# Optimization experiments

Hardware: AMD Instinct MI355X
Metric: run time of the kernel (lower is better)

The kernel has to match this reference:

```python
import jax, jax.numpy as jnp
import numpy as np

N_NODES = 100000
N_EDGES = 3200000
IN_CH = 128
HID = 8
HEADS = 8
NEG_SLOPE = 0.2  # PyG GATConv default


def setup_inputs() -> dict:
    key = jax.random.key(0)
    ks = jax.random.split(key, 12)
    s = 0.1
    return {
        "x": jax.random.normal(ks[0], (N_NODES, IN_CH), jnp.float32),
        "edge_index": jax.random.randint(ks[1], (2, N_EDGES), 0, N_NODES, dtype=jnp.int64),
        "W1": jax.random.normal(ks[2], (IN_CH, HEADS * HID), jnp.float32) * s,
        "a_src1": jax.random.normal(ks[3], (1, HEADS, HID), jnp.float32) * s,
        "a_dst1": jax.random.normal(ks[4], (1, HEADS, HID), jnp.float32) * s,
        "b1": jax.random.normal(ks[5], (HEADS * HID,), jnp.float32) * s,
        "W2": jax.random.normal(ks[6], (HEADS * HID, HID), jnp.float32) * s,
        "a_src2": jax.random.normal(ks[7], (1, 1, HID), jnp.float32) * s,
        "a_dst2": jax.random.normal(ks[8], (1, 1, HID), jnp.float32) * s,
        "b2": jax.random.normal(ks[9], (HID,), jnp.float32) * s,
        "Wc": jax.random.normal(ks[10], (HID, 2), jnp.float32) * s,
        "bc": jax.random.normal(ks[11], (2,), jnp.float32) * s,
    }


def gat_conv(x, src, dst, W, a_src, a_dst, b, concat):
    """PyG-style GATConv (eval mode, self-loops already appended to src/dst)."""
    n = x.shape[0]
    H, C = a_src.shape[1], a_src.shape[2]
    h = (x @ W).reshape(n, H, C)                       # [N,H,C]
    alpha_src = jnp.sum(h * a_src, axis=-1)            # [N,H]
    alpha_dst = jnp.sum(h * a_dst, axis=-1)            # [N,H]
    e = jax.nn.leaky_relu(alpha_src[src] + alpha_dst[dst], NEG_SLOPE)  # [E,H]
    # segment softmax over destination-node neighborhoods
    m = jax.ops.segment_max(e, dst, num_segments=n)    # [N,H]
    m = jnp.where(jnp.isfinite(m), m, 0.0)
    p = jnp.exp(e - m[dst])
    z = jax.ops.segment_sum(p, dst, num_segments=n)    # [N,H]
    alpha = p / (z[dst] + 1e-16)                       # [E,H]
    out = jax.ops.segment_sum(alpha[..., None] * h[src], dst, num_segments=n)  # [N,H,C]
    out = out.reshape(n, H * C) if concat else out.mean(axis=1)
    return out + b


def reference(x, edge_index, W1, a_src1, a_dst1, b1, W2, a_src2, a_dst2, b2, Wc, bc):
    n = x.shape[0]
    loops = jnp.arange(n, dtype=edge_index.dtype)
    src = jnp.concatenate([edge_index[0], loops])
    dst = jnp.concatenate([edge_index[1], loops])
    h = jax.nn.relu(gat_conv(x, src, dst, W1, a_src1, a_dst1, b1, concat=True))
    embeddings = gat_conv(h, src, dst, W2, a_src2, a_dst2, b2, concat=False)
    logits = embeddings @ Wc + bc
    return embeddings, logits
```

## Files before the change

### kernel.cpp

```cpp
#include <hip/hip_runtime.h>
#include <hip/hip_bf16.h>
#include <hip/hip_fp16.h>

#define NN 100000
#define IN_CH 128
#define HID 8
#define HEADS 8
#define HC 64
#define BSH 8
#define NBUCK ((NN + 255) >> 8)
#define NBLK 512
#define PCAP 10240
#define LOG2E 1.44269504088896340736f
#define QSCALE (8.0f / 127.0f)
#define QINV   (127.0f / 8.0f)

__device__ __forceinline__ unsigned short f2bf(float f) {
    unsigned u = __float_as_uint(f);
    unsigned r = (u + 0x7fffu + ((u >> 16) & 1u)) >> 16;
    return (unsigned short)r;
}


__global__ __launch_bounds__(256) void k_bincount(const int* __restrict__ ei, int E, int ET,
                                                  int cpb, int* __restrict__ cnt) {
    __shared__ int h[NBUCK];
    for (int i = threadIdx.x; i < NBUCK; i += 256) h[i] = 0;
    __syncthreads();
    int beg = blockIdx.x * cpb, end = min(ET, beg + cpb);
    for (int t = beg + threadIdx.x; t < end; t += 256) {
        int d = (t < E) ? ei[E + t] : (t - E);
        atomicAdd(&h[d >> BSH], 1);
    }
    __syncthreads();
    for (int i = threadIdx.x; i < NBUCK; i += 256) cnt[i * NBLK + blockIdx.x] = h[i];
}

__global__ __launch_bounds__(256) void k_colscan(int* __restrict__ cnt, int* __restrict__ btot) {
    __shared__ int sd[256];
    int t = threadIdx.x;
    int* col = cnt + blockIdx.x * NBLK;
    int v0 = col[2 * t], v1 = col[2 * t + 1];
    int s = v0 + v1;
    sd[t] = s;
    __syncthreads();
    for (int off = 1; off < 256; off <<= 1) {
        int u = (t >= off) ? sd[t - off] : 0;
        __syncthreads();
        sd[t] += u;
        __syncthreads();
    }
    int excl = sd[t] - s;
    col[2 * t] = excl;
    col[2 * t + 1] = excl + v0;
    if (t == 255) btot[blockIdx.x] = excl + s;
}

__global__ __launch_bounds__(256) void k_bucketbase(const int* __restrict__ btot,
                                                    int* __restrict__ bbase,
                                                    int* __restrict__ row_ptr) {
    __shared__ int sd[256];
    int t = threadIdx.x;
    int v0 = (2 * t < NBUCK) ? btot[2 * t] : 0;
    int v1 = (2 * t + 1 < NBUCK) ? btot[2 * t + 1] : 0;
    int s = v0 + v1;
    sd[t] = s;
    __syncthreads();
    for (int off = 1; off < 256; off <<= 1) {
        int u = (t >= off) ? sd[t - off] : 0;
        __syncthreads();
        sd[t] += u;
        __syncthreads();
    }
    int excl = sd[t] - s;
    if (2 * t < NBUCK) bbase[2 * t] = excl;
    if (2 * t + 1 < NBUCK) bbase[2 * t + 1] = excl + v0;
    if (t == 255) { bbase[NBUCK] = excl + s; row_ptr[NN] = excl + s; }
}

__global__ __launch_bounds__(256) void k_binscatter(const int* __restrict__ ei, int E, int ET,
                                                    int cpb, const int* __restrict__ cnt,
                                                    const int* __restrict__ bbase,
                                                    unsigned* __restrict__ pairs) {
    __shared__ int cur[NBUCK];
    for (int i = threadIdx.x; i < NBUCK; i += 256)
        cur[i] = bbase[i] + cnt[i * NBLK + blockIdx.x];
    __syncthreads();
    int beg = blockIdx.x * cpb, end = min(ET, beg + cpb);
    for (int t = beg + threadIdx.x; t < end; t += 256) {
        int s, d;
        if (t < E) { s = ei[t]; d = ei[E + t]; } else { s = t - E; d = t - E; }
        int pos = atomicAdd(&cur[d >> BSH], 1);
        pairs[pos] = ((unsigned)s << 8) | (unsigned)(d & 255);
    }
}

__global__ __launch_bounds__(256) void k_bucketscatter(const unsigned* __restrict__ pairs,
                                                       const int* __restrict__ bbase,
                                                       int* __restrict__ row_ptr,
                                                       int* __restrict__ csr) {
    __shared__ unsigned pl[PCAP];
    __shared__ int h[256];
    __shared__ int sd[256];
    int b = blockIdx.x;
    int t = threadIdx.x;
    int beg = bbase[b], end = bbase[b + 1];
    int cntE = end - beg;
    bool inl = cntE <= PCAP;
    if (inl)
        for (int j = t; j < cntE; j += 256) pl[j] = pairs[beg + j];
    h[t] = 0;
    __syncthreads();
    for (int j = t; j < cntE; j += 256) {
        unsigned pv = inl ? pl[j] : pairs[beg + j];
        atomicAdd(&h[pv & 255u], 1);
    }
    __syncthreads();
    int v = h[t];
    sd[t] = v;
    __syncthreads();
    for (int off = 1; off < 256; off <<= 1) {
        int u = (t >= off) ? sd[t - off] : 0;
        __syncthreads();
        sd[t] += u;
        __syncthreads();
    }
    int excl = sd[t] - v;
    int node = (b << 8) + t;
    if (node < NN) row_ptr[node] = beg + excl;
    __syncthreads();
    h[t] = beg + excl;
    __syncthreads();
    for (int j = t; j < cntE; j += 256) {
        unsigned pv = inl ? pl[j] : pairs[beg + j];
        int pos = atomicAdd(&h[pv & 255u], 1);
        csr[pos] = (int)(pv >> 8);
    }
}


__global__ __launch_bounds__(256) void k_gemm1(const float* __restrict__ x,
                                               const float* __restrict__ W1,
                                               const float* __restrict__ aS,
                                               const float* __restrict__ aD,
                                               unsigned* __restrict__ h1q,
                                               unsigned short* __restrict__ asrc1h,
                                               float* __restrict__ adst1) {
    __shared__ float wl[IN_CH * HC];
    int tid = threadIdx.x;
    {
        const float4* Wg4 = (const float4*)W1;
        float4* wl4 = (float4*)wl;
#pragma unroll
        for (int i = 0; i < 8; ++i) wl4[tid + i * 256] = Wg4[tid + i * 256];
    }
    __syncthreads();
    int lane = tid & 63;
    int wv = tid >> 6;
    int q = lane >> 4;
    int c0 = (lane & 15) * 4;
    int base = blockIdx.x * 64 + wv * 16 + q * 4;
    if (base + 4 > NN) base = NN - 4;
    const float4* xr0 = (const float4*)(x + (size_t)(base + 0) * IN_CH);
    const float4* xr1 = (const float4*)(x + (size_t)(base + 1) * IN_CH);
    const float4* xr2 = (const float4*)(x + (size_t)(base + 2) * IN_CH);
    const float4* xr3 = (const float4*)(x + (size_t)(base + 3) * IN_CH);
    float4 ac0 = make_float4(0.f, 0.f, 0.f, 0.f);
    float4 ac1 = ac0, ac2 = ac0, ac3 = ac0;
#pragma unroll 2
    for (int kq = 0; kq < IN_CH / 4; ++kq) {
        const float4* wrow = (const float4*)(wl + (kq * 4) * HC + c0);
        float4 w0 = wrow[0];
        float4 w1 = wrow[HC / 4];
        float4 w2 = wrow[2 * (HC / 4)];
        float4 w3 = wrow[3 * (HC / 4)];
        float4 xv;
        xv = xr0[kq];
        ac0.x += xv.x * w0.x + xv.y * w1.x + xv.z * w2.x + xv.w * w3.x;
        ac0.y += xv.x * w0.y + xv.y * w1.y + xv.z * w2.y + xv.w * w3.y;
        ac0.z += xv.x * w0.z + xv.y * w1.z + xv.z * w2.z + xv.w * w3.z;
        ac0.w += xv.x * w0.w + xv.y * w1.w + xv.z * w2.w + xv.w * w3.w;
        xv = xr1[kq];
        ac1.x += xv.x * w0.x + xv.y * w1.x + xv.z * w2.x + xv.w * w3.x;
        ac1.y += xv.x * w0.y + xv.y * w1.y + xv.z * w2.y + xv.w * w3.y;
        ac1.z += xv.x * w0.z + xv.y * w1.z + xv.z * w2.z + xv.w * w3.z;
        ac1.w += xv.x * w0.w + xv.y * w1.w + xv.z * w2.w + xv.w * w3.w;
        xv = xr2[kq];
        ac2.x += xv.x * w0.x + xv.y * w1.x + xv.z * w2.x + xv.w * w3.x;
        ac2.y += xv.x * w0.y + xv.y * w1.y + xv.z * w2.y + xv.w * w3.y;
        ac2.z += xv.x * w0.z + xv.y * w1.z + xv.z * w2.z + xv.w * w3.z;
        ac2.w += xv.x * w0.w + xv.y * w1.w + xv.z * w2.w + xv.w * w3.w;
        xv = xr3[kq];
        ac3.x += xv.x * w0.x + xv.y * w1.x + xv.z * w2.x + xv.w * w3.x;
        ac3.y += xv.x * w0.y + xv.y * w1.y + xv.z * w2.y + xv.w * w3.y;
        ac3.z += xv.x * w0.z + xv.y * w1.z + xv.z * w2.z + xv.w * w3.z;
        ac3.w += xv.x * w0.w + xv.y * w1.w + xv.z * w2.w + xv.w * w3.w;
    }
    float4 accs[4] = {ac0, ac1, ac2, ac3};
#pragma unroll
    for (int r = 0; r < 4; ++r) {
        float4 acc = accs[r];
        int row = base + r;
        int q0 = min(max(__float2int_rn(acc.x * QINV) + 128, 0), 255);
        int q1 = min(max(__float2int_rn(acc.y * QINV) + 128, 0), 255);
        int q2 = min(max(__float2int_rn(acc.z * QINV) + 128, 0), 255);
        int q3 = min(max(__float2int_rn(acc.w * QINV) + 128, 0), 255);
        unsigned u = (unsigned)q0 | ((unsigned)q1 << 8) | ((unsigned)q2 << 16) |
                     ((unsigned)q3 << 24);
        h1q[row * 16 + (lane & 15)] = u;
        int head = (lane & 15) >> 1;
        int cl = c0 & 7;
        const float* as = aS + head * 8 + cl;
        const float* ad = aD + head * 8 + cl;
        float ps = acc.x * as[0] + acc.y * as[1] + acc.z * as[2] + acc.w * as[3];
        float pd = acc.x * ad[0] + acc.y * ad[1] + acc.z * ad[2] + acc.w * ad[3];
        ps += __shfl_xor(ps, 1, 64);
        pd += __shfl_xor(pd, 1, 64);
        if ((lane & 1) == 0) {
            asrc1h[row * 8 + head] = __half_as_ushort(__float2half(ps * LOG2E));
            adst1[row * 8 + head] = pd * LOG2E;
        }
    }
}


__global__ __launch_bounds__(256) void k_agg1(const int* __restrict__ row_ptr,
                                              const int* __restrict__ csr,
                                              const unsigned short* __restrict__ asrc1h,
                                              const float* __restrict__ adst1,
                                              const uint2* __restrict__ h1q,
                                              const float* __restrict__ b1,
                                              const float* __restrict__ W2,
                                              const float* __restrict__ aS2,
                                              const float* __restrict__ aD2,
                                              unsigned short* __restrict__ h2bf,
                                              float* __restrict__ asrc2,
                                              float* __restrict__ adst2) {
    int tid = threadIdx.x;
    int lane = tid & 63;
    int slot = lane >> 3;
    int hl = lane & 7;
    float w2r[8];
#pragma unroll
    for (int i = 0; i < 8; ++i) w2r[i] = W2[(hl * 8 + i) * 8 + slot];
    float4 b0 = *(const float4*)(b1 + hl * 8);
    float4 b1v = *(const float4*)(b1 + hl * 8 + 4);
    float as2 = aS2[slot], ad2 = aD2[slot];
    int nbase = (blockIdx.x * 4 + (tid >> 6)) * 4;
    for (int ni = 0; ni < 4; ++ni) {
        int n = nbase + ni;
        float adst = adst1[n * 8 + hl];
        int beg = row_ptr[n], end = row_ptr[n + 1];
        int nit = (end - beg + 7) >> 3;
        float z = 0.f;
        float4 accA = make_float4(0.f, 0.f, 0.f, 0.f);
        float4 accB = make_float4(0.f, 0.f, 0.f, 0.f);
        int j0 = beg + slot;
        bool v0 = j0 < end;
        int s0 = v0 ? csr[j0] : 0;
        int j1 = j0 + 8;
        bool v1 = j1 < end;
        int s1 = v1 ? csr[j1] : 0;
        unsigned short a0 = asrc1h[s0 * 8 + hl];
        uint2 r0 = h1q[s0 * 8 + hl];
        int jn = j1;
        for (int it = 0; it < nit; ++it) {
            int j2 = jn + 8;
            bool v2 = j2 < end;
            int s2 = v2 ? csr[j2] : 0;
            unsigned short a1 = asrc1h[s1 * 8 + hl];
            uint2 r1 = h1q[s1 * 8 + hl];
            float e = __half2float(__ushort_as_half(a0)) + adst;
            e = fmaxf(e, 0.2f * e);
            float p = v0 ? exp2f(e) : 0.f;
            z += p;
            accA.x += p * (float)(r0.x & 255u);
            accA.y += p * (float)((r0.x >> 8) & 255u);
            accA.z += p * (float)((r0.x >> 16) & 255u);
            accA.w += p * (float)(r0.x >> 24);
            accB.x += p * (float)(r0.y & 255u);
            accB.y += p * (float)((r0.y >> 8) & 255u);
            accB.z += p * (float)((r0.y >> 16) & 255u);
            accB.w += p * (float)(r0.y >> 24);
            v0 = v1; a0 = a1; r0 = r1;
            v1 = v2; s1 = s2;
            jn = j2;
        }
#pragma unroll
        for (int off = 8; off <= 32; off <<= 1) {
            z += __shfl_xor(z, off, 64);
            accA.x += __shfl_xor(accA.x, off, 64);
            accA.y += __shfl_xor(accA.y, off, 64);
            accA.z += __shfl_xor(accA.z, off, 64);
            accA.w += __shfl_xor(accA.w, off, 64);
            accB.x += __shfl_xor(accB.x, off, 64);
            accB.y += __shfl_xor(accB.y, off, 64);
            accB.z += __shfl_xor(accB.z, off, 64);
            accB.w += __shfl_xor(accB.w, off, 64);
        }
        float inv = 1.f / (z + 1e-16f);
        float si = QSCALE * inv;
        float zc = 128.f * z;
        float hr0 = fmaxf((accA.x - zc) * si + b0.x, 0.f);
        float hr1 = fmaxf((accA.y - zc) * si + b0.y, 0.f);
        float hr2 = fmaxf((accA.z - zc) * si + b0.z, 0.f);
        float hr3 = fmaxf((accA.w - zc) * si + b0.w, 0.f);
        float hr4 = fmaxf((accB.x - zc) * si + b1v.x, 0.f);
        float hr5 = fmaxf((accB.y - zc) * si + b1v.y, 0.f);
        float hr6 = fmaxf((accB.z - zc) * si + b1v.z, 0.f);
        float hr7 = fmaxf((accB.w - zc) * si + b1v.w, 0.f);
        float part = hr0 * w2r[0] + hr1 * w2r[1] + hr2 * w2r[2] + hr3 * w2r[3] +
                     hr4 * w2r[4] + hr5 * w2r[5] + hr6 * w2r[6] + hr7 * w2r[7];
        part += __shfl_xor(part, 1, 64);
        part += __shfl_xor(part, 2, 64);
        part += __shfl_xor(part, 4, 64);
        if (hl == 0) {
            h2bf[n * 8 + slot] = f2bf(part);
            float s2v = part * as2;
            float d2v = part * ad2;
            s2v += __shfl_xor(s2v, 8, 64);
            s2v += __shfl_xor(s2v, 16, 64);
            s2v += __shfl_xor(s2v, 32, 64);
            d2v += __shfl_xor(d2v, 8, 64);
            d2v += __shfl_xor(d2v, 16, 64);
            d2v += __shfl_xor(d2v, 32, 64);
            if (slot == 0) {
                asrc2[n] = s2v * LOG2E;
                adst2[n] = d2v * LOG2E;
            }
        }
    }
}


__global__ __launch_bounds__(256) void k_agg2(const int* __restrict__ row_ptr,
                                              const int* __restrict__ csr,
                                              const float* __restrict__ asrc2,
                                              const float* __restrict__ adst2,
                                              const unsigned short* __restrict__ h2bf,
                                              const float* __restrict__ b2,
                                              const float* __restrict__ Wc,
                                              const float* __restrict__ bc,
                                              float* __restrict__ out) {
    int tid = threadIdx.x;
    int lane = tid & 63;
    int slot = lane >> 3;
    int sl = lane & 7;
    float b2v = b2[sl];
    float wc0 = Wc[sl * 2 + 0], wc1 = Wc[sl * 2 + 1];
    int nbase = (blockIdx.x * 4 + (tid >> 6)) * 4;
    for (int ni = 0; ni < 4; ++ni) {
        int n = nbase + ni;
        float adst = adst2[n];
        int beg = row_ptr[n], end = row_ptr[n + 1];
        int nit = (end - beg + 7) >> 3;
        float z = 0.f, acc = 0.f;
        int j0 = beg + slot;
        bool v0 = j0 < end;
        int s0 = v0 ? csr[j0] : 0;
        int j1 = j0 + 8;
        bool v1 = j1 < end;
        int s1 = v1 ? csr[j1] : 0;
        float a0 = asrc2[s0];
        unsigned short u0 = h2bf[s0 * 8 + sl];
        int jn = j1;
        for (int it = 0; it < nit; ++it) {
            int j2 = jn + 8;
            bool v2 = j2 < end;
            int s2 = v2 ? csr[j2] : 0;
            float a1 = asrc2[s1];
            unsigned short u1 = h2bf[s1 * 8 + sl];
            float e = a0 + adst;
            e = fmaxf(e, 0.2f * e);
            float p = v0 ? exp2f(e) : 0.f;
            float h0 = __uint_as_float(((unsigned)u0) << 16);
            z += p;
            acc += p * h0;
            v0 = v1; a0 = a1; u0 = u1;
            v1 = v2; s1 = s2;
            jn = j2;
        }
#pragma unroll
        for (int off = 8; off <= 32; off <<= 1) {
            z += __shfl_xor(z, off, 64);
            acc += __shfl_xor(acc, off, 64);
        }
        float emb = acc / (z + 1e-16f) + b2v;
        if (slot == 0) out[(size_t)n * HID + sl] = emb;
        float t0 = emb * wc0;
        float t1 = emb * wc1;
        t0 += __shfl_xor(t0, 1, 64); t0 += __shfl_xor(t0, 2, 64); t0 += __shfl_xor(t0, 4, 64);
        t1 += __shfl_xor(t1, 1, 64); t1 += __shfl_xor(t1, 2, 64); t1 += __shfl_xor(t1, 4, 64);
        if (lane == 0) {
            out[(size_t)NN * HID + n * 2 + 0] = t0 + bc[0];
            out[(size_t)NN * HID + n * 2 + 1] = t1 + bc[1];
        }
    }
}


extern "C" void kernel_launch(void* const* d_in, const int* in_sizes, int n_in,
                              void* d_out, int out_size, void* d_ws, size_t ws_size,
                              hipStream_t stream) {
    const float* x  = (const float*)d_in[0];
    const int*   ei = (const int*)d_in[1];
    const float* W1 = (const float*)d_in[2];
    const float* aS = (const float*)d_in[3];
    const float* aD = (const float*)d_in[4];
    const float* b1 = (const float*)d_in[5];
    const float* W2 = (const float*)d_in[6];
    const float* aS2 = (const float*)d_in[7];
    const float* aD2 = (const float*)d_in[8];
    const float* b2 = (const float*)d_in[9];
    const float* Wc = (const float*)d_in[10];
    const float* bc = (const float*)d_in[11];

    int E = in_sizes[1] / 2;
    int N = NN;
    int ET = E + N;
    int cpb = (ET + NBLK - 1) / NBLK;

    char* p = (char*)d_ws;
    auto alloc = [&](size_t bytes) -> char* {
        char* r = p;
        p += (bytes + 255) & ~(size_t)255;
        return r;
    };
    unsigned* h1q   = (unsigned*)alloc((size_t)N * 16 * 4);
    unsigned short* asrc1h = (unsigned short*)alloc((size_t)N * 8 * 2);
    float* adst1    = (float*)alloc((size_t)N * 8 * 4);
    unsigned short* h2bf = (unsigned short*)alloc((size_t)N * 8 * 2);
    float* asrc2    = (float*)alloc((size_t)N * 4);
    float* adst2    = (float*)alloc((size_t)N * 4);
    int*   row_ptr  = (int*)alloc((size_t)(N + 1) * 4);
    int*   cnt      = (int*)alloc((size_t)NBUCK * NBLK * 4);
    int*   btot     = (int*)alloc((size_t)NBUCK * 4);
    int*   bbase    = (int*)alloc((size_t)(NBUCK + 1) * 4);
    int*   csr      = (int*)alloc((size_t)ET * 4);
    unsigned* pairs = (unsigned*)alloc((size_t)ET * 4);

    k_bincount<<<NBLK, 256, 0, stream>>>(ei, E, ET, cpb, cnt);
    k_colscan<<<NBUCK, 256, 0, stream>>>(cnt, btot);
    k_bucketbase<<<1, 256, 0, stream>>>(btot, bbase, row_ptr);
    k_binscatter<<<NBLK, 256, 0, stream>>>(ei, E, ET, cpb, cnt, bbase, pairs);
    k_bucketscatter<<<NBUCK, 256, 0, stream>>>(pairs, bbase, row_ptr, csr);

    k_gemm1<<<(N + 63) / 64, 256, 0, stream>>>(x, W1, aS, aD, h1q, asrc1h, adst1);
    k_agg1<<<N / 16, 256, 0, stream>>>(row_ptr, csr, asrc1h, adst1,
                                       (const uint2*)h1q, b1, W2, aS2, aD2,
                                       h2bf, asrc2, adst2);
    k_agg2<<<N / 16, 256, 0, stream>>>(row_ptr, csr, asrc2, adst2, h2bf, b2, Wc, bc,
                                       (float*)d_out);
}
```

Measured before the change: 216.3 us.

## Co-schedule GEMM1 blocks with CSR-build kernels and drop validity checks in aggregation

Merges the layer-1 GEMM into the bincount and binscatter kernels as extra blocks, splitting the GEMM rows between the two launches. This lets the compute-bound GEMM overlap the atomic-heavy CSR construction and removes one kernel launch. The shared-memory buffer is reused by both roles, so the bincount/binscatter blocks now reserve the full 32KB GEMM allocation, which may lower their occupancy. Separately, the aggregation loops load sentinel attention scores (-inf half, or -3e38 float) for invalid edges so exp2 yields zero, removing the per-edge validity select.

```diff
diff --git a/kernel.cpp b/kernel.cpp
--- a/kernel.cpp
+++ b/kernel.cpp
@@ -11,6 +11,9 @@
 #define NBUCK ((NN + 255) >> 8)
 #define NBLK 512
 #define PCAP 10240
+#define GB  ((NN + 63) / 64)
+#define GH1 782
+#define GH2 (GB - GH1)
 #define LOG2E 1.44269504088896340736f
 #define QSCALE (8.0f / 127.0f)
 #define QINV   (127.0f / 8.0f)
@@ -22,131 +25,15 @@
 }
 
 
-__global__ __launch_bounds__(256) void k_bincount(const int* __restrict__ ei, int E, int ET,
-                                                  int cpb, int* __restrict__ cnt) {
-    __shared__ int h[NBUCK];
-    for (int i = threadIdx.x; i < NBUCK; i += 256) h[i] = 0;
-    __syncthreads();
-    int beg = blockIdx.x * cpb, end = min(ET, beg + cpb);
-    for (int t = beg + threadIdx.x; t < end; t += 256) {
-        int d = (t < E) ? ei[E + t] : (t - E);
-        atomicAdd(&h[d >> BSH], 1);
-    }
-    __syncthreads();
-    for (int i = threadIdx.x; i < NBUCK; i += 256) cnt[i * NBLK + blockIdx.x] = h[i];
-}
-
-__global__ __launch_bounds__(256) void k_colscan(int* __restrict__ cnt, int* __restrict__ btot) {
-    __shared__ int sd[256];
-    int t = threadIdx.x;
-    int* col = cnt + blockIdx.x * NBLK;
-    int v0 = col[2 * t], v1 = col[2 * t + 1];
-    int s = v0 + v1;
-    sd[t] = s;
-    __syncthreads();
-    for (int off = 1; off < 256; off <<= 1) {
-        int u = (t >= off) ? sd[t - off] : 0;
-        __syncthreads();
-        sd[t] += u;
-        __syncthreads();
-    }
-    int excl = sd[t] - s;
-    col[2 * t] = excl;
-    col[2 * t + 1] = excl + v0;
-    if (t == 255) btot[blockIdx.x] = excl + s;
-}
-
-__global__ __launch_bounds__(256) void k_bucketbase(const int* __restrict__ btot,
-                                                    int* __restrict__ bbase,
-                                                    int* __restrict__ row_ptr) {
-    __shared__ int sd[256];
-    int t = threadIdx.x;
-    int v0 = (2 * t < NBUCK) ? btot[2 * t] : 0;
-    int v1 = (2 * t + 1 < NBUCK) ? btot[2 * t + 1] : 0;
-    int s = v0 + v1;
-    sd[t] = s;
-    __syncthreads();
-    for (int off = 1; off < 256; off <<= 1) {
-        int u = (t >= off) ? sd[t - off] : 0;
-        __syncthreads();
-        sd[t] += u;
-        __syncthreads();
-    }
-    int excl = sd[t] - s;
-    if (2 * t < NBUCK) bbase[2 * t] = excl;
-    if (2 * t + 1 < NBUCK) bbase[2 * t + 1] = excl + v0;
-    if (t == 255) { bbase[NBUCK] = excl + s; row_ptr[NN] = excl + s; }
-}
-
-__global__ __launch_bounds__(256) void k_binscatter(const int* __restrict__ ei, int E, int ET,
-                                                    int cpb, const int* __restrict__ cnt,
-                                                    const int* __restrict__ bbase,
-                                                    unsigned* __restrict__ pairs) {
-    __shared__ int cur[NBUCK];
-    for (int i = threadIdx.x; i < NBUCK; i += 256)
-        cur[i] = bbase[i] + cnt[i * NBLK + blockIdx.x];
-    __syncthreads();
-    int beg = blockIdx.x * cpb, end = min(ET, beg + cpb);
-    for (int t = beg + threadIdx.x; t < end; t += 256) {
-        int s, d;
-        if (t < E) { s = ei[t]; d = ei[E + t]; } else { s = t - E; d = t - E; }
-        int pos = atomicAdd(&cur[d >> BSH], 1);
-        pairs[pos] = ((unsigned)s << 8) | (unsigned)(d & 255);
-    }
-}
-
-__global__ __launch_bounds__(256) void k_bucketscatter(const unsigned* __restrict__ pairs,
-                                                       const int* __restrict__ bbase,
-                                                       int* __restrict__ row_ptr,
-                                                       int* __restrict__ csr) {
-    __shared__ unsigned pl[PCAP];
-    __shared__ int h[256];
-    __shared__ int sd[256];
-    int b = blockIdx.x;
-    int t = threadIdx.x;
-    int beg = bbase[b], end = bbase[b + 1];
-    int cntE = end - beg;
-    bool inl = cntE <= PCAP;
-    if (inl)
-        for (int j = t; j < cntE; j += 256) pl[j] = pairs[beg + j];
-    h[t] = 0;
-    __syncthreads();
-    for (int j = t; j < cntE; j += 256) {
-        unsigned pv = inl ? pl[j] : pairs[beg + j];
-        atomicAdd(&h[pv & 255u], 1);
-    }
-    __syncthreads();
-    int v = h[t];
-    sd[t] = v;
-    __syncthreads();
-    for (int off = 1; off < 256; off <<= 1) {
-        int u = (t >= off) ? sd[t - off] : 0;
-        __syncthreads();
-        sd[t] += u;
-        __syncthreads();
-    }
-    int excl = sd[t] - v;
-    int node = (b << 8) + t;
-    if (node < NN) row_ptr[node] = beg + excl;
-    __syncthreads();
-    h[t] = beg + excl;
-    __syncthreads();
-    for (int j = t; j < cntE; j += 256) {
-        unsigned pv = inl ? pl[j] : pairs[beg + j];
-        int pos = atomicAdd(&h[pv & 255u], 1);
-        csr[pos] = (int)(pv >> 8);
-    }
-}
-
-
-__global__ __launch_bounds__(256) void k_gemm1(const float* __restrict__ x,
-                                               const float* __restrict__ W1,
-                                               const float* __restrict__ aS,
-                                               const float* __restrict__ aD,
-                                               unsigned* __restrict__ h1q,
-                                               unsigned short* __restrict__ asrc1h,
-                                               float* __restrict__ adst1) {
-    __shared__ float wl[IN_CH * HC];
+__device__ __forceinline__ void gemm1_body(int bid,
+                                           const float* __restrict__ x,
+                                           const float* __restrict__ W1,
+                                           const float* __restrict__ aS,
+                                           const float* __restrict__ aD,
+                                           unsigned* __restrict__ h1q,
+                                           unsigned short* __restrict__ asrc1h,
+                                           float* __restrict__ adst1,
+                                           float* wl) {
     int tid = threadIdx.x;
     {
         const float4* Wg4 = (const float4*)W1;
@@ -159,7 +46,7 @@
     int wv = tid >> 6;
     int q = lane >> 4;
     int c0 = (lane & 15) * 4;
-    int base = blockIdx.x * 64 + wv * 16 + q * 4;
+    int base = bid * 64 + wv * 16 + q * 4;
     if (base + 4 > NN) base = NN - 4;
     const float4* xr0 = (const float4*)(x + (size_t)(base + 0) * IN_CH);
     const float4* xr1 = (const float4*)(x + (size_t)(base + 1) * IN_CH);
@@ -220,6 +107,148 @@
             asrc1h[row * 8 + head] = __half_as_ushort(__float2half(ps * LOG2E));
             adst1[row * 8 + head] = pd * LOG2E;
         }
+    }
+}
+
+
+__global__ __launch_bounds__(256) void k_f1(const int* __restrict__ ei, int E, int ET, int cpb,
+                                            int* __restrict__ cnt,
+                                            const float* __restrict__ x,
+                                            const float* __restrict__ W1,
+                                            const float* __restrict__ aS,
+                                            const float* __restrict__ aD,
+                                            unsigned* __restrict__ h1q,
+                                            unsigned short* __restrict__ asrc1h,
+                                            float* __restrict__ adst1) {
+    __shared__ float smem[IN_CH * HC];
+    if (blockIdx.x < NBLK) {
+        int* h = (int*)smem;
+        for (int i = threadIdx.x; i < NBUCK; i += 256) h[i] = 0;
+        __syncthreads();
+        int beg = blockIdx.x * cpb, end = min(ET, beg + cpb);
+        for (int t = beg + threadIdx.x; t < end; t += 256) {
+            int d = (t < E) ? ei[E + t] : (t - E);
+            atomicAdd(&h[d >> BSH], 1);
+        }
+        __syncthreads();
+        for (int i = threadIdx.x; i < NBUCK; i += 256) cnt[i * NBLK + blockIdx.x] = h[i];
+    } else {
+        gemm1_body(blockIdx.x - NBLK, x, W1, aS, aD, h1q, asrc1h, adst1, smem);
+    }
+}
+
+__global__ __launch_bounds__(256) void k_colscan(int* __restrict__ cnt, int* __restrict__ btot) {
+    __shared__ int sd[256];
+    int t = threadIdx.x;
+    int* col = cnt + blockIdx.x * NBLK;
+    int v0 = col[2 * t], v1 = col[2 * t + 1];
+    int s = v0 + v1;
+    sd[t] = s;
+    __syncthreads();
+    for (int off = 1; off < 256; off <<= 1) {
+        int u = (t >= off) ? sd[t - off] : 0;
+        __syncthreads();
+        sd[t] += u;
+        __syncthreads();
+    }
+    int excl = sd[t] - s;
+    col[2 * t] = excl;
+    col[2 * t + 1] = excl + v0;
+    if (t == 255) btot[blockIdx.x] = excl + s;
+}
+
+__global__ __launch_bounds__(256) void k_bucketbase(const int* __restrict__ btot,
+                                                    int* __restrict__ bbase,
+                                                    int* __restrict__ row_ptr) {
+    __shared__ int sd[256];
+    int t = threadIdx.x;
+    int v0 = (2 * t < NBUCK) ? btot[2 * t] : 0;
+    int v1 = (2 * t + 1 < NBUCK) ? btot[2 * t + 1] : 0;
+    int s = v0 + v1;
+    sd[t] = s;
+    __syncthreads();
+    for (int off = 1; off < 256; off <<= 1) {
+        int u = (t >= off) ? sd[t - off] : 0;
+        __syncthreads();
+        sd[t] += u;
+        __syncthreads();
+    }
+    int excl = sd[t] - s;
+    if (2 * t < NBUCK) bbase[2 * t] = excl;
+    if (2 * t + 1 < NBUCK) bbase[2 * t + 1] = excl + v0;
+    if (t == 255) { bbase[NBUCK] = excl + s; row_ptr[NN] = excl + s; }
+}
+
+
+__global__ __launch_bounds__(256) void k_f2(const int* __restrict__ ei, int E, int ET, int cpb,
+                                            const int* __restrict__ cnt,
+                                            const int* __restrict__ bbase,
+                                            unsigned* __restrict__ pairs,
+                                            const float* __restrict__ x,
+                                            const float* __restrict__ W1,
+                                            const float* __restrict__ aS,
+                                            const float* __restrict__ aD,
+                                            unsigned* __restrict__ h1q,
+                                            unsigned short* __restrict__ asrc1h,
+                                            float* __restrict__ adst1) {
+    __shared__ float smem[IN_CH * HC];
+    if (blockIdx.x < NBLK) {
+        int* cur = (int*)smem;
+        for (int i = threadIdx.x; i < NBUCK; i += 256)
+            cur[i] = bbase[i] + cnt[i * NBLK + blockIdx.x];
+        __syncthreads();
+        int beg = blockIdx.x * cpb, end = min(ET, beg + cpb);
+        for (int t = beg + threadIdx.x; t < end; t += 256) {
+            int s, d;
+            if (t < E) { s = ei[t]; d = ei[E + t]; } else { s = t - E; d = t - E; }
+            int pos = atomicAdd(&cur[d >> BSH], 1);
+            pairs[pos] = ((unsigned)s << 8) | (unsigned)(d & 255);
+        }
+    } else {
+        gemm1_body(blockIdx.x - NBLK + GH1, x, W1, aS, aD, h1q, asrc1h, adst1, smem);
+    }
+}
+
+__global__ __launch_bounds__(256) void k_bucketscatter(const unsigned* __restrict__ pairs,
+                                                       const int* __restrict__ bbase,
+                                                       int* __restrict__ row_ptr,
+                                                       int* __restrict__ csr) {
+    __shared__ unsigned pl[PCAP];
+    __shared__ int h[256];
+    __shared__ int sd[256];
+    int b = blockIdx.x;
+    int t = threadIdx.x;
+    int beg = bbase[b], end = bbase[b + 1];
+    int cntE = end - beg;
+    bool inl = cntE <= PCAP;
+    if (inl)
+        for (int j = t; j < cntE; j += 256) pl[j] = pairs[beg + j];
+    h[t] = 0;
+    __syncthreads();
+    for (int j = t; j < cntE; j += 256) {
+        unsigned pv = inl ? pl[j] : pairs[beg + j];
+        atomicAdd(&h[pv & 255u], 1);
+    }
+    __syncthreads();
+    int v = h[t];
+    sd[t] = v;
+    __syncthreads();
+    for (int off = 1; off < 256; off <<= 1) {
+        int u = (t >= off) ? sd[t - off] : 0;
+        __syncthreads();
+        sd[t] += u;
+        __syncthreads();
+    }
+    int excl = sd[t] - v;
+    int node = (b << 8) + t;
+    if (node < NN) row_ptr[node] = beg + excl;
+    __syncthreads();
+    h[t] = beg + excl;
+    __syncthreads();
+    for (int j = t; j < cntE; j += 256) {
+        unsigned pv = inl ? pl[j] : pairs[beg + j];
+        int pos = atomicAdd(&h[pv & 255u], 1);
+        csr[pos] = (int)(pv >> 8);
     }
 }
 
@@ -261,18 +290,18 @@
         int j1 = j0 + 8;
         bool v1 = j1 < end;
         int s1 = v1 ? csr[j1] : 0;
-        unsigned short a0 = asrc1h[s0 * 8 + hl];
+        unsigned short a0 = v0 ? asrc1h[s0 * 8 + hl] : (unsigned short)0xFC00u;
         uint2 r0 = h1q[s0 * 8 + hl];
         int jn = j1;
         for (int it = 0; it < nit; ++it) {
             int j2 = jn + 8;
             bool v2 = j2 < end;
             int s2 = v2 ? csr[j2] : 0;
-            unsigned short a1 = asrc1h[s1 * 8 + hl];
+            unsigned short a1 = v1 ? asrc1h[s1 * 8 + hl] : (unsigned short)0xFC00u;
             uint2 r1 = h1q[s1 * 8 + hl];
             float e = __half2float(__ushort_as_half(a0)) + adst;
             e = fmaxf(e, 0.2f * e);
-            float p = v0 ? exp2f(e) : 0.f;
+            float p = exp2f(e);
             z += p;
             accA.x += p * (float)(r0.x & 255u);
             accA.y += p * (float)((r0.x >> 8) & 255u);
@@ -282,7 +311,7 @@
             accB.y += p * (float)((r0.y >> 8) & 255u);
             accB.z += p * (float)((r0.y >> 16) & 255u);
             accB.w += p * (float)(r0.y >> 24);
-            v0 = v1; a0 = a1; r0 = r1;
+            a0 = a1; r0 = r1;
             v1 = v2; s1 = s2;
             jn = j2;
         }
@@ -361,22 +390,22 @@
         int j1 = j0 + 8;
         bool v1 = j1 < end;
         int s1 = v1 ? csr[j1] : 0;
-        float a0 = asrc2[s0];
+        float a0 = v0 ? asrc2[s0] : -3.0e38f;
         unsigned short u0 = h2bf[s0 * 8 + sl];
         int jn = j1;
         for (int it = 0; it < nit; ++it) {
             int j2 = jn + 8;
             bool v2 = j2 < end;
             int s2 = v2 ? csr[j2] : 0;
-            float a1 = asrc2[s1];
+            float a1 = v1 ? asrc2[s1] : -3.0e38f;
             unsigned short u1 = h2bf[s1 * 8 + sl];
             float e = a0 + adst;
             e = fmaxf(e, 0.2f * e);
-            float p = v0 ? exp2f(e) : 0.f;
+            float p = exp2f(e);
             float h0 = __uint_as_float(((unsigned)u0) << 16);
             z += p;
             acc += p * h0;
-            v0 = v1; a0 = a1; u0 = u1;
+            a0 = a1; u0 = u1;
             v1 = v2; s1 = s2;
             jn = j2;
         }
@@ -439,13 +468,14 @@
     int*   csr      = (int*)alloc((size_t)ET * 4);
     unsigned* pairs = (unsigned*)alloc((size_t)ET * 4);
 
-    k_bincount<<<NBLK, 256, 0, stream>>>(ei, E, ET, cpb, cnt);
+    k_f1<<<NBLK + GH1, 256, 0, stream>>>(ei, E, ET, cpb, cnt,
+                                         x, W1, aS, aD, h1q, asrc1h, adst1);
     k_colscan<<<NBUCK, 256, 0, stream>>>(cnt, btot);
     k_bucketbase<<<1, 256, 0, stream>>>(btot, bbase, row_ptr);
-    k_binscatter<<<NBLK, 256, 0, stream>>>(ei, E, ET, cpb, cnt, bbase, pairs);
+    k_f2<<<NBLK + GH2, 256, 0, stream>>>(ei, E, ET, cpb, cnt, bbase, pairs,
+                                         x, W1, aS, aD, h1q, asrc1h, adst1);
     k_bucketscatter<<<NBUCK, 256, 0, stream>>>(pairs, bbase, row_ptr, csr);
 
-    k_gemm1<<<(N + 63) / 64, 256, 0, stream>>>(x, W1, aS, aD, h1q, asrc1h, adst1);
     k_agg1<<<N / 16, 256, 0, stream>>>(row_ptr, csr, asrc1h, adst1,
                                        (const uint2*)h1q, b1, W2, aS2, aD2,
                                        h2bf, asrc2, adst2);
```

Measured after the change: 227.0 us. +5.0%, slower.
